# Optimization experiments

Hardware: AMD Instinct MI355X
Metric: run time of the kernel (lower is better)

## Reference

```python
import jax, jax.numpy as jnp
import numpy as np
from jax import lax

K = 11        # kernel_size
SIGMA = 2.0   # gaussian sigma
N_T = 20      # max diffusion timestep
C = 3         # channels

# torchvision GaussianBlur 1D kernel: pdf = exp(-0.5*(x/sigma)^2), normalized
_x = np.linspace(-(K - 1) / 2.0, (K - 1) / 2.0, K)
_pdf = np.exp(-0.5 * (_x / SIGMA) ** 2)
_k1d = (_pdf / _pdf.sum()).astype(np.float32)
# depthwise separable kernels: [C,1,K,1] and [C,1,1,K] (OIHW, feature_group_count=C)
W_H = jnp.asarray(np.tile(_k1d.reshape(1, 1, K, 1), (C, 1, 1, 1)))
W_W = jnp.asarray(np.tile(_k1d.reshape(1, 1, 1, K), (C, 1, 1, 1)))
DN = ('NCHW', 'OIHW', 'NCHW')
PAD = K // 2


def _blur(z):
    # reflect padding as torchvision GaussianBlur, then separable depthwise conv
    zp = jnp.pad(z, ((0, 0), (0, 0), (PAD, PAD), (0, 0)), mode='reflect')
    zp = lax.conv_general_dilated(zp, W_H, (1, 1), 'VALID',
                                  dimension_numbers=DN, feature_group_count=C)
    zp = jnp.pad(zp, ((0, 0), (0, 0), (0, 0), (PAD, PAD)), mode='reflect')
    return lax.conv_general_dilated(zp, W_W, (1, 1), 'VALID',
                                    dimension_numbers=DN, feature_group_count=C)


def setup_inputs() -> dict:
    key = jax.random.key(0)
    kx, kt = jax.random.split(key)
    x = jax.random.normal(kx, (64, 3, 256, 256), dtype=jnp.float32)
    t = jax.random.randint(kt, (64,), 1, N_T, dtype=jnp.int32)
    return {'x': x, 't': t}


def reference(x, t):
    # batch_blur: sample i gets blurred t[i] times. Vectorized as N_T masked
    # blur steps: at step i, samples with t > i take the blurred value.
    mask_keep = t[:, None, None, None]  # [B,1,1,1]

    def step(z, i):
        zb = _blur(z)
        z = jnp.where(mask_keep > i, zb, z)
        return z, None

    z_t, _ = lax.scan(step, x, jnp.arange(N_T))
    return z_t
```

## Files before the change

### kernel.cpp

```cpp
#include <hip/hip_runtime.h>

#define IMG 65536
#define W 256
#define H 256
#define RMAX 40


__global__ __launch_bounds__(256) void init_kernel(const int* __restrict__ t,
                                                   float* __restrict__ ktab,
                                                   int* __restrict__ ord,
                                                   int* __restrict__ rtab) {
  __shared__ double cur[256];
  __shared__ double sc[256];
  __shared__ double base[11];
  __shared__ int keys[192];
  __shared__ int sRmax;
  int tid = threadIdx.x;
  int tt = blockIdx.x;
  if (tid == 0) {
    double p[11];
    double s = 0.0;
    for (int i = 0; i < 11; ++i) {
      double xx = (double)(i - 5) * 0.5;
      p[i] = exp(-0.5 * xx * xx);
      s += p[i];
    }
    for (int i = 0; i < 11; ++i) base[i] = (double)(float)(p[i] / s);
  }
  __syncthreads();

  if (tt == 0) {
    ktab[tid] = (tid == 8) ? 1.0f : 0.0f;
    if (tid == 0) rtab[0] = 0;
    if (tid < 192) keys[tid] = min(max(t[tid / 3], 0), 19);
    __syncthreads();
    if (tid < 192) {
      int k = keys[tid];
      int rank = 0;
      for (int j = 0; j < 192; ++j) {
        int kj = keys[j];
        if (kj > k || (kj == k && j < tid)) ++rank;
      }
      ord[rank] = tid;
    }
    return;
  }

  cur[tid] = (tid < 11) ? base[tid] : 0.0;
  __syncthreads();
  for (int step = 2; step <= tt; ++step) {
    int Lprev = 10 * (step - 1) + 1;
    double a = 0.0;
    for (int i = 0; i < 11; ++i) {
      int jj = tid - i;
      if (jj >= 0 && jj < Lprev) a += base[i] * cur[jj];
    }
    __syncthreads();
    cur[tid] = a;
    __syncthreads();
  }
  sc[tid] = cur[tid];
  __syncthreads();
#pragma unroll
  for (int off = 1; off < 256; off <<= 1) {
    double tmp = (tid >= off) ? sc[tid - off] : 0.0;
    __syncthreads();
    sc[tid] += tmp;
    __syncthreads();
  }
  if (tid == 0) sRmax = 1;
  __syncthreads();
  int c = 5 * tt;
  double total = sc[255];
  if (tid >= 1 && tid <= c) {
    double Srm1 = sc[c + tid - 1] - sc[c - tid];
    if (total - Srm1 > 1e-5) atomicMax(&sRmax, tid);
  }
  __syncthreads();
  int Rk = min(sRmax, RMAX);
  double ksum = sc[c + Rk] - ((c - Rk - 1 >= 0) ? sc[c - Rk - 1] : 0.0);
  double scale = 1.0 / ksum;
  if (tid == 0) rtab[tt] = Rk;
  int c0 = c - Rk;
  int Lk = 2 * Rk + 1;
  ktab[tt * 256 + tid] =
      (tid >= 8 && tid < 8 + Lk) ? (float)(cur[tid - 8 + c0] * scale) : 0.0f;
}

__global__ __launch_bounds__(256, 6) void hpass_kernel(const float* __restrict__ x,
                                                       const int* __restrict__ t,
                                                       const float* __restrict__ ktab,
                                                       const int* __restrict__ ord,
                                                       const int* __restrict__ rtab,
                                                       float* __restrict__ out) {
  __shared__ float tile[352 * 17];
  __shared__ float ktile[256];
  int tid = threadIdx.x;
  int img = __builtin_amdgcn_readfirstlane(ord[blockIdx.y]);
  int wt = blockIdx.x;
  int b = img / 3;
  int tv = __builtin_amdgcn_readfirstlane(min(max(t[b], 0), 19));
  int R = __builtin_amdgcn_readfirstlane(rtab[tv]);
  int L = 2 * R + 1;
  const float* __restrict__ kt = ktab + tv * 256;
  const float* src = x + (size_t)img * IMG + (wt << 4);
  float* dst = out + (size_t)img * IMG + (wt << 4);
  ktile[tid] = kt[tid];
  {
    int c4 = (tid & 3) << 2;
    int r0 = tid >> 2;
#pragma unroll
    for (int i = 0; i < 6; ++i) {
      int rr = r0 + (i << 6);
      if (rr < 352) {
        int p = rr - RMAX;
        int srow = 255 - abs(255 - abs(p));
        float4 v = *reinterpret_cast<const float4*>(src + srow * W + c4);
        tile[rr * 17 + c4 + 0] = v.x;
        tile[rr * 17 + c4 + 1] = v.y;
        tile[rr * 17 + c4 + 2] = v.z;
        tile[rr * 17 + c4 + 3] = v.w;
      }
    }
  }
  __syncthreads();
  int col = tid & 15;
  int rgrp = tid >> 4;
  int nIter = (L + 30) & ~15;
  int h0 = rgrp << 4;
  float acc[16];
  float kq[16];
#pragma unroll
  for (int o = 0; o < 16; ++o) { acc[o] = 0.f; kq[o] = 0.f; }
  int pb = h0 - R + RMAX;
  for (int jb = 0; jb < nIter; jb += 16) {
#pragma unroll
    for (int u = 0; u < 16; ++u) {
      kq[u] = ktile[jb + u + 8];
      float v = tile[(pb + jb + u) * 17 + col];
#pragma unroll
      for (int o = 0; o < 16; ++o) acc[o] += kq[(u - o) & 15] * v;
    }
  }
#pragma unroll
  for (int o = 0; o < 16; ++o) dst[(h0 + o) * W + col] = acc[o];
}

__global__ __launch_bounds__(256, 3) void wpass_split(const float* __restrict__ srcbuf,
                                                      const int* __restrict__ t,
                                                      const float* __restrict__ ktab,
                                                      const int* __restrict__ ord,
                                                      const int* __restrict__ rtab,
                                                      float* __restrict__ dstbuf) {
  __shared__ float tile[32 * 361];
  __shared__ float ktile[256];
  int tid = threadIdx.x;
  int img = __builtin_amdgcn_readfirstlane(ord[blockIdx.y]);
  int ht = blockIdx.x;
  int b = img / 3;
  int tv = __builtin_amdgcn_readfirstlane(min(max(t[b], 0), 19));
  int R = __builtin_amdgcn_readfirstlane(rtab[tv]);
  int L = 2 * R + 1;
  const float* __restrict__ kt = ktab + tv * 256;
  const float* src = srcbuf + (size_t)img * IMG + (ht << 5) * W;
  float* dst = dstbuf + (size_t)img * IMG + (ht << 5) * W;
  ktile[tid] = kt[tid];
  {
    int srow = tid >> 3;
    int jbase = tid & 7;
    const float* sp = src + srow * W;
    float* tp0 = &tile[srow * 361];
#pragma unroll
    for (int k = 0; k < 11; ++k) {
      int j = jbase + (k << 3);
      int c0 = -RMAX + (j << 2);
      float* tp = tp0 + c0 + RMAX;
      if (c0 >= 0 && c0 <= 252) {
        float4 v = *reinterpret_cast<const float4*>(sp + c0);
        tp[0] = v.x; tp[1] = v.y; tp[2] = v.z; tp[3] = v.w;
      } else {
#pragma unroll
        for (int d = 0; d < 4; ++d) {
          int cc = c0 + d;
          int rc = 255 - abs(255 - abs(cc));
          tp[d] = sp[rc];
        }
      }
    }
  }
  __syncthreads();
  int row = tid & 31;
  int wgrp = tid >> 5;
  int rowbase = row * 361;
  int nIter = (L + 30) & ~15;
  for (int g = 0; g < 2; ++g) {
    int w0 = (wgrp << 5) + (g << 4);
    float acc[16];
    float kq[16];
#pragma unroll
    for (int o = 0; o < 16; ++o) { acc[o] = 0.f; kq[o] = 0.f; }
    int pb = w0 - R + RMAX;
    for (int jb = 0; jb < nIter; jb += 16) {
#pragma unroll
      for (int u = 0; u < 16; ++u) {
        kq[u] = ktile[jb + u + 8];
        float v = tile[rowbase + pb + jb + u];
#pragma unroll
        for (int o = 0; o < 16; ++o) acc[o] += kq[(u - o) & 15] * v;
      }
    }
    float4 v0 = make_float4(acc[0], acc[1], acc[2], acc[3]);
    float4 v1 = make_float4(acc[4], acc[5], acc[6], acc[7]);
    float4 v2 = make_float4(acc[8], acc[9], acc[10], acc[11]);
    float4 v3 = make_float4(acc[12], acc[13], acc[14], acc[15]);
    float* o0 = dst + row * W + w0;
    *reinterpret_cast<float4*>(o0 + 0) = v0;
    *reinterpret_cast<float4*>(o0 + 4) = v1;
    *reinterpret_cast<float4*>(o0 + 8) = v2;
    *reinterpret_cast<float4*>(o0 + 12) = v3;
  }
}

__global__ __launch_bounds__(256, 3) void wpass_inplace(const int* __restrict__ t,
                                                        const float* __restrict__ ktab,
                                                        const int* __restrict__ ord,
                                                        const int* __restrict__ rtab,
                                                        float* __restrict__ io) {
  __shared__ float tile[32 * 361];
  __shared__ float ktile[256];
  int tid = threadIdx.x;
  int img = __builtin_amdgcn_readfirstlane(ord[blockIdx.y]);
  int ht = blockIdx.x;
  int b = img / 3;
  int tv = __builtin_amdgcn_readfirstlane(min(max(t[b], 0), 19));
  int R = __builtin_amdgcn_readfirstlane(rtab[tv]);
  int L = 2 * R + 1;
  const float* __restrict__ kt = ktab + tv * 256;
  float* base = io + (size_t)img * IMG + (ht << 5) * W;
  ktile[tid] = kt[tid];
  {
    int srow = tid >> 3;
    int jbase = tid & 7;
    const float* sp = base + srow * W;
    float* tp0 = &tile[srow * 361];
#pragma unroll
    for (int k = 0; k < 11; ++k) {
      int j = jbase + (k << 3);
      int c0 = -RMAX + (j << 2);
      float* tp = tp0 + c0 + RMAX;
      if (c0 >= 0 && c0 <= 252) {
        float4 v = *reinterpret_cast<const float4*>(sp + c0);
        tp[0] = v.x; tp[1] = v.y; tp[2] = v.z; tp[3] = v.w;
      } else {
#pragma unroll
        for (int d = 0; d < 4; ++d) {
          int cc = c0 + d;
          int rc = 255 - abs(255 - abs(cc));
          tp[d] = sp[rc];
        }
      }
    }
  }
  __syncthreads();
  int row = tid & 31;
  int wgrp = tid >> 5;
  int rowbase = row * 361;
  int nIter = (L + 30) & ~15;
  for (int g = 0; g < 2; ++g) {
    int w0 = (wgrp << 5) + (g << 4);
    float acc[16];
    float kq[16];
#pragma unroll
    for (int o = 0; o < 16; ++o) { acc[o] = 0.f; kq[o] = 0.f; }
    int pb = w0 - R + RMAX;
    for (int jb = 0; jb < nIter; jb += 16) {
#pragma unroll
      for (int u = 0; u < 16; ++u) {
        kq[u] = ktile[jb + u + 8];
        float v = tile[rowbase + pb + jb + u];
#pragma unroll
        for (int o = 0; o < 16; ++o) acc[o] += kq[(u - o) & 15] * v;
      }
    }
    float4 v0 = make_float4(acc[0], acc[1], acc[2], acc[3]);
    float4 v1 = make_float4(acc[4], acc[5], acc[6], acc[7]);
    float4 v2 = make_float4(acc[8], acc[9], acc[10], acc[11]);
    float4 v3 = make_float4(acc[12], acc[13], acc[14], acc[15]);
    float* o0 = base + row * W + w0;
    *reinterpret_cast<float4*>(o0 + 0) = v0;
    *reinterpret_cast<float4*>(o0 + 4) = v1;
    *reinterpret_cast<float4*>(o0 + 8) = v2;
    *reinterpret_cast<float4*>(o0 + 12) = v3;
  }
}

extern "C" void kernel_launch(void* const* d_in, const int* in_sizes, int n_in,
                              void* d_out, int out_size, void* d_ws, size_t ws_size,
                              hipStream_t stream) {
  const float* x = (const float*)d_in[0];
  const int* t = (const int*)d_in[1];
  float* out = (float*)d_out;
  float* ktab = (float*)d_ws;
  int* ord = (int*)((char*)d_ws + 20480);
  int* rtab = (int*)((char*)d_ws + 21248);
  const size_t mid_off = 32768;
  const size_t mid_bytes = (size_t)192 * IMG * 4;

  hipLaunchKernelGGL(init_kernel, dim3(20), dim3(256), 0, stream, t, ktab, ord, rtab);
  if (ws_size >= mid_off + mid_bytes) {
    float* mid = (float*)((char*)d_ws + mid_off);
    hipLaunchKernelGGL(hpass_kernel, dim3(16, 192), dim3(256), 0, stream, x, t, ktab, ord, rtab, mid);
    hipLaunchKernelGGL(wpass_split, dim3(8, 192), dim3(256), 0, stream, mid, t, ktab, ord, rtab, out);
  } else {
    hipLaunchKernelGGL(hpass_kernel, dim3(16, 192), dim3(256), 0, stream, x, t, ktab, ord, rtab, out);
    hipLaunchKernelGGL(wpass_inplace, dim3(8, 192), dim3(256), 0, stream, t, ktab, ord, rtab, out);
  }
}
```

Measured before the change: 93.38 us.

## Restructure vertical blur pass with 32-column transposed swizzled tile and dual accumulators

Result: faster. 80.36 us (median of 2 runs) (-13.9%).

```diff
diff --git a/kernel.cpp b/kernel.cpp
--- a/kernel.cpp
+++ b/kernel.cpp
@@ -87,14 +87,13 @@
       (tid >= 8 && tid < 8 + Lk) ? (float)(cur[tid - 8 + c0] * scale) : 0.0f;
 }
 
-__global__ __launch_bounds__(256, 6) void hpass_kernel(const float* __restrict__ x,
+__global__ __launch_bounds__(256, 3) void hpass_kernel(const float* __restrict__ x,
                                                        const int* __restrict__ t,
                                                        const float* __restrict__ ktab,
                                                        const int* __restrict__ ord,
                                                        const int* __restrict__ rtab,
                                                        float* __restrict__ out) {
-  __shared__ float tile[352 * 17];
-  __shared__ float ktile[256];
+  __shared__ float tile[32 * 352];
   int tid = threadIdx.x;
   int img = __builtin_amdgcn_readfirstlane(ord[blockIdx.y]);
   int wt = blockIdx.x;
@@ -102,48 +101,66 @@
   int tv = __builtin_amdgcn_readfirstlane(min(max(t[b], 0), 19));
   int R = __builtin_amdgcn_readfirstlane(rtab[tv]);
   int L = 2 * R + 1;
-  const float* __restrict__ kt = ktab + tv * 256;
-  const float* src = x + (size_t)img * IMG + (wt << 4);
-  float* dst = out + (size_t)img * IMG + (wt << 4);
-  ktile[tid] = kt[tid];
+  int d = (RMAX - R) & 3;
+  const float* __restrict__ kt = ktab + tv * 256 + (8 - d);
+  const float* src = x + (size_t)img * IMG + (wt << 5);
+  float* dst = out + (size_t)img * IMG + (wt << 5);
   {
-    int c4 = (tid & 3) << 2;
-    int r0 = tid >> 2;
-#pragma unroll
-    for (int i = 0; i < 6; ++i) {
-      int rr = r0 + (i << 6);
-      if (rr < 352) {
-        int p = rr - RMAX;
-        int srow = 255 - abs(255 - abs(p));
-        float4 v = *reinterpret_cast<const float4*>(src + srow * W + c4);
-        tile[rr * 17 + c4 + 0] = v.x;
-        tile[rr * 17 + c4 + 1] = v.y;
-        tile[rr * 17 + c4 + 2] = v.z;
-        tile[rr * 17 + c4 + 3] = v.w;
-      }
-    }
-  }
-  __syncthreads();
-  int col = tid & 15;
-  int rgrp = tid >> 4;
-  int nIter = (L + 30) & ~15;
+    int c4 = (tid & 7) << 2;
+    int r0 = tid >> 3;
+#pragma unroll
+    for (int i = 0; i < 11; ++i) {
+      int rr = r0 + (i << 5);
+      int p = rr - RMAX;
+      int srow = 255 - abs(255 - abs(p));
+      float4 v = *reinterpret_cast<const float4*>(src + srow * W + c4);
+      int rc = rr & ~3, rl = rr & 3;
+      tile[(c4 + 0) * 352 + (rc ^ (((c4 + 0) & 7) << 2)) + rl] = v.x;
+      tile[(c4 + 1) * 352 + (rc ^ (((c4 + 1) & 7) << 2)) + rl] = v.y;
+      tile[(c4 + 2) * 352 + (rc ^ (((c4 + 2) & 7) << 2)) + rl] = v.z;
+      tile[(c4 + 3) * 352 + (rc ^ (((c4 + 3) & 7) << 2)) + rl] = v.w;
+    }
+  }
+  __syncthreads();
+  int col = tid & 31;
+  int rgrp = tid >> 5;
   int h0 = rgrp << 4;
-  float acc[16];
-  float kq[16];
-#pragma unroll
-  for (int o = 0; o < 16; ++o) { acc[o] = 0.f; kq[o] = 0.f; }
-  int pb = h0 - R + RMAX;
+  int nIter = (L + d + 30) & ~15;
+  int A = h0 + ((RMAX - R) & ~3);
+  int cb = col * 352;
+  int swz = (col & 7) << 2;
+  float accA[16], accB[16], kq[16];
+#pragma unroll
+  for (int o = 0; o < 16; ++o) { accA[o] = 0.f; accB[o] = 0.f; kq[o] = 0.f; }
   for (int jb = 0; jb < nIter; jb += 16) {
+    float kn[16];
+#pragma unroll
+    for (int u = 0; u < 16; ++u) kn[u] = kt[jb + u];
+    float va[16], vb[16];
+#pragma unroll
+    for (int m = 0; m < 4; ++m) {
+      int qa = A + jb + (m << 2);
+      float4 ta = *reinterpret_cast<const float4*>(&tile[cb + (qa ^ swz)]);
+      float4 tb = *reinterpret_cast<const float4*>(&tile[cb + ((qa + 128) ^ swz)]);
+      va[4 * m + 0] = ta.x; va[4 * m + 1] = ta.y; va[4 * m + 2] = ta.z; va[4 * m + 3] = ta.w;
+      vb[4 * m + 0] = tb.x; vb[4 * m + 1] = tb.y; vb[4 * m + 2] = tb.z; vb[4 * m + 3] = tb.w;
+    }
 #pragma unroll
     for (int u = 0; u < 16; ++u) {
-      kq[u] = ktile[jb + u + 8];
-      float v = tile[(pb + jb + u) * 17 + col];
-#pragma unroll
-      for (int o = 0; o < 16; ++o) acc[o] += kq[(u - o) & 15] * v;
-    }
-  }
-#pragma unroll
-  for (int o = 0; o < 16; ++o) dst[(h0 + o) * W + col] = acc[o];
+      kq[u] = kn[u];
+#pragma unroll
+      for (int o = 0; o < 16; ++o) {
+        float k = kq[(u - o) & 15];
+        accA[o] += k * va[u];
+        accB[o] += k * vb[u];
+      }
+    }
+  }
+#pragma unroll
+  for (int o = 0; o < 16; ++o) {
+    dst[(h0 + o) * W + col] = accA[o];
+    dst[(h0 + 128 + o) * W + col] = accB[o];
+  }
 }
 
 __global__ __launch_bounds__(256, 3) void wpass_split(const float* __restrict__ srcbuf,
@@ -236,12 +253,12 @@
   int R = __builtin_amdgcn_readfirstlane(rtab[tv]);
   int L = 2 * R + 1;
   const float* __restrict__ kt = ktab + tv * 256;
-  float* base = io + (size_t)img * IMG + (ht << 5) * W;
+  float* basep = io + (size_t)img * IMG + (ht << 5) * W;
   ktile[tid] = kt[tid];
   {
     int srow = tid >> 3;
     int jbase = tid & 7;
-    const float* sp = base + srow * W;
+    const float* sp = basep + srow * W;
     float* tp0 = &tile[srow * 361];
 #pragma unroll
     for (int k = 0; k < 11; ++k) {
@@ -286,7 +303,7 @@
     float4 v1 = make_float4(acc[4], acc[5], acc[6], acc[7]);
     float4 v2 = make_float4(acc[8], acc[9], acc[10], acc[11]);
     float4 v3 = make_float4(acc[12], acc[13], acc[14], acc[15]);
-    float* o0 = base + row * W + w0;
+    float* o0 = basep + row * W + w0;
     *reinterpret_cast<float4*>(o0 + 0) = v0;
     *reinterpret_cast<float4*>(o0 + 4) = v1;
     *reinterpret_cast<float4*>(o0 + 8) = v2;
@@ -309,10 +326,10 @@
   hipLaunchKernelGGL(init_kernel, dim3(20), dim3(256), 0, stream, t, ktab, ord, rtab);
   if (ws_size >= mid_off + mid_bytes) {
     float* mid = (float*)((char*)d_ws + mid_off);
-    hipLaunchKernelGGL(hpass_kernel, dim3(16, 192), dim3(256), 0, stream, x, t, ktab, ord, rtab, mid);
+    hipLaunchKernelGGL(hpass_kernel, dim3(8, 192), dim3(256), 0, stream, x, t, ktab, ord, rtab, mid);
     hipLaunchKernelGGL(wpass_split, dim3(8, 192), dim3(256), 0, stream, mid, t, ktab, ord, rtab, out);
   } else {
-    hipLaunchKernelGGL(hpass_kernel, dim3(16, 192), dim3(256), 0, stream, x, t, ktab, ord, rtab, out);
+    hipLaunchKernelGGL(hpass_kernel, dim3(8, 192), dim3(256), 0, stream, x, t, ktab, ord, rtab, out);
     hipLaunchKernelGGL(wpass_inplace, dim3(8, 192), dim3(256), 0, stream, t, ktab, ord, rtab, out);
   }
 }
```
